# Optimization experiments

Hardware: AMD Instinct MI355X
Metric: run time of the kernel (lower is better)

The kernel has to match this reference:

```python
import jax, jax.numpy as jnp
import numpy as np

N_NODES = 100000


def _add_self_loops(edge_index, n):
    loop = jnp.arange(n, dtype=edge_index.dtype)
    src = jnp.concatenate([edge_index[0], loop])
    dst = jnp.concatenate([edge_index[1], loop])
    return src, dst


def gcn_conv(x, edge_index, W, b):
    # x: [N, Fin], edge_index: [2, E]; PyG GCNConv with add_self_loops + symmetric norm
    n = x.shape[0]
    src, dst = _add_self_loops(edge_index, n)
    # degree of augmented graph (counting incoming edges at dst, weight 1)
    deg = jax.ops.segment_sum(jnp.ones_like(dst, dtype=x.dtype), dst, num_segments=n)
    dinv = jnp.where(deg > 0, jax.lax.rsqrt(deg), 0.0)
    norm = dinv[src] * dinv[dst]                      # [E+N]
    h = x @ W                                         # [N, Fout] (transform first: Fout small)
    msg = h[src] * norm[:, None]                      # gather + scale
    out = jax.ops.segment_sum(msg, dst, num_segments=n)  # scatter-add
    return out + b


def setup_inputs() -> dict:
    key = jax.random.key(0)
    k1, k2, k3, k4, k5, k6 = jax.random.split(key, 6)
    F_in, H, C = 512, 16, 40
    x = jax.random.normal(k1, (N_NODES, F_in), dtype=jnp.float32)
    edge_index = jax.random.randint(k2, (2, 3200000), 0, N_NODES, dtype=jnp.int64)
    s1 = 1.0 / np.sqrt(F_in)
    s2 = 1.0 / np.sqrt(H)
    W1 = jax.random.uniform(k3, (F_in, H), jnp.float32, -s1, s1)
    b1 = jax.random.uniform(k4, (H,), jnp.float32, -s1, s1)
    W2 = jax.random.uniform(k5, (H, C), jnp.float32, -s2, s2)
    b2 = jax.random.uniform(k6, (C,), jnp.float32, -s2, s2)
    return {"x": x, "edge_index": edge_index, "W1": W1, "b1": b1, "W2": W2, "b2": b2}


def reference(x, edge_index, W1, b1, W2, b2):
    h = gcn_conv(x, edge_index, W1, b1)
    h = jax.nn.relu(h)
    # F.dropout(training=False) -> identity at inference
    h = gcn_conv(h, edge_index, W2, b2)
    return jax.nn.log_softmax(h, axis=1)
```

## Files before the change

kernel.cpp:

```cpp
#include <hip/hip_runtime.h>

#define N_NODES 100000
#define N_EDGES 3200000
#define FIN 512
#define FH 16
#define FC 40
#define NB_N ((N_NODES + 255) / 256)
#define NBKT 391
#define NBLK_P 256
#define CHUNK (N_EDGES / NBLK_P)


__global__ __launch_bounds__(256) void kA1(const int* __restrict__ dst,
                                           int* __restrict__ H) {
  __shared__ int h[NBKT];
  int t = threadIdx.x;
  for (int i = t; i < NBKT; i += 256) h[i] = 0;
  __syncthreads();
  int base = blockIdx.x * CHUNK;
  for (int i = t; i < CHUNK; i += 256) atomicAdd(&h[dst[base + i] >> 8], 1);
  __syncthreads();
  for (int i = t; i < NBKT; i += 256) H[blockIdx.x * NBKT + i] = h[i];
}


__global__ __launch_bounds__(256) void kA2(const int* __restrict__ H,
                                           int* __restrict__ P,
                                           int* __restrict__ T) {
  __shared__ int s[256];
  int t = threadIdx.x, b = blockIdx.x;
  int v = H[t * NBKT + b];
  s[t] = v;
  __syncthreads();
  for (int d = 1; d < 256; d <<= 1) {
    int x = (t >= d) ? s[t - d] : 0;
    __syncthreads();
    s[t] += x;
    __syncthreads();
  }
  P[t * NBKT + b] = s[t] - v;
  if (t == 255) T[b] = s[t];
}


__global__ __launch_bounds__(512) void kA3s(const int* __restrict__ T,
                                            int* __restrict__ Base,
                                            int* __restrict__ off) {
  __shared__ int s[512];
  int t = threadIdx.x;
  int v = (t < NBKT) ? T[t] : 0;
  s[t] = v;
  __syncthreads();
  for (int d = 1; d < 512; d <<= 1) {
    int x = (t >= d) ? s[t - d] : 0;
    __syncthreads();
    s[t] += x;
    __syncthreads();
  }
  if (t < NBKT) Base[t] = s[t] - v;
  if (t == 0) off[N_NODES] = N_EDGES;
}


__global__ __launch_bounds__(256) void kA3(const int* __restrict__ ei,
                                           const int* __restrict__ Base,
                                           const int* __restrict__ P,
                                           int* __restrict__ stage) {
  __shared__ int cur[NBKT];
  int t = threadIdx.x, blk = blockIdx.x;
  for (int i = t; i < NBKT; i += 256) cur[i] = Base[i] + P[blk * NBKT + i];
  __syncthreads();
  int base = blk * CHUNK;
  for (int i = t; i < CHUNK; i += 256) {
    int s = ei[base + i];
    int d = ei[N_EDGES + base + i];
    int slot = atomicAdd(&cur[d >> 8], 1);
    stage[slot] = s | ((d & 255) << 17);
  }
}


__global__ __launch_bounds__(256) void kB(const int* __restrict__ stage,
                                          const int* __restrict__ Base,
                                          const int* __restrict__ T,
                                          int* __restrict__ off,
                                          int* __restrict__ csr,
                                          float* __restrict__ dinv) {
  __shared__ int hist[256], cursor[256], sc[256];
  int t = threadIdx.x, b = blockIdx.x;
  int base = Base[b], cnt = T[b];
  hist[t] = 0;
  __syncthreads();
  for (int i = t; i < cnt; i += 256) atomicAdd(&hist[stage[base + i] >> 17], 1);
  __syncthreads();
  int c = hist[t];
  sc[t] = c;
  __syncthreads();
  for (int d = 1; d < 256; d <<= 1) {
    int x = (t >= d) ? sc[t - d] : 0;
    __syncthreads();
    sc[t] += x;
    __syncthreads();
  }
  int excl = sc[t] - c;
  int node = b * 256 + t;
  if (node < N_NODES) {
    off[node] = base + excl;
    dinv[node] = rsqrtf((float)(c + 1));
  }
  cursor[t] = excl;
  __syncthreads();
  for (int i = t; i < cnt; i += 256) {
    int pk = stage[base + i];
    int slot = atomicAdd(&cursor[pk >> 17], 1);
    csr[base + slot] = pk & 0x1FFFF;
  }
}


__global__ __launch_bounds__(256) void k_gemm1(const float* __restrict__ x,
                                               const float* __restrict__ W1,
                                               const float* __restrict__ dinv,
                                               float* __restrict__ p1) {
  __shared__ float xs[256 * 36];
  const int t = threadIdx.x;
  const int row0 = blockIdx.x * 256;
  const int row = row0 + t;
  float acc[FH];
#pragma unroll
  for (int c = 0; c < FH; c++) acc[c] = 0.0f;

  for (int kc = 0; kc < FIN; kc += 32) {
    float4 ld[8];
#pragma unroll
    for (int i = 0; i < 8; i++) {
      int idx = t + 256 * i;
      int r = idx >> 3, c4 = idx & 7;
      int gr = row0 + r;
      ld[i] = (gr < N_NODES)
                  ? *(const float4*)(x + (size_t)gr * FIN + kc + c4 * 4)
                  : make_float4(0.f, 0.f, 0.f, 0.f);
    }
    __syncthreads();
#pragma unroll
    for (int i = 0; i < 8; i++) {
      int idx = t + 256 * i;
      int r = idx >> 3, c4 = idx & 7;
      *(float4*)(&xs[r * 36 + c4 * 4]) = ld[i];
    }
    __syncthreads();
    float4 xr[8];
#pragma unroll
    for (int q = 0; q < 8; q++) xr[q] = *(const float4*)(&xs[t * 36 + q * 4]);
    const float4* w4 = (const float4*)(W1 + (size_t)kc * FH);
#pragma unroll
    for (int k = 0; k < 32; k++) {
      float xv = ((const float*)xr)[k];
      float4 wa = w4[k * 4 + 0], wb = w4[k * 4 + 1];
      float4 wc = w4[k * 4 + 2], wd = w4[k * 4 + 3];
      acc[0] = fmaf(xv, wa.x, acc[0]);   acc[1] = fmaf(xv, wa.y, acc[1]);
      acc[2] = fmaf(xv, wa.z, acc[2]);   acc[3] = fmaf(xv, wa.w, acc[3]);
      acc[4] = fmaf(xv, wb.x, acc[4]);   acc[5] = fmaf(xv, wb.y, acc[5]);
      acc[6] = fmaf(xv, wb.z, acc[6]);   acc[7] = fmaf(xv, wb.w, acc[7]);
      acc[8] = fmaf(xv, wc.x, acc[8]);   acc[9] = fmaf(xv, wc.y, acc[9]);
      acc[10] = fmaf(xv, wc.z, acc[10]); acc[11] = fmaf(xv, wc.w, acc[11]);
      acc[12] = fmaf(xv, wd.x, acc[12]); acc[13] = fmaf(xv, wd.y, acc[13]);
      acc[14] = fmaf(xv, wd.z, acc[14]); acc[15] = fmaf(xv, wd.w, acc[15]);
    }
  }

  if (row < N_NODES) {
    float dv = dinv[row];
#pragma unroll
    for (int c = 0; c < FH; c++) acc[c] *= dv;
#pragma unroll
    for (int q = 0; q < 4; q++)
      *(float4*)(p1 + (size_t)row * FH + q * 4) = ((const float4*)acc)[q];
  }
}


__global__ __launch_bounds__(256) void k_gather1(const int* __restrict__ off,
                                                 const int* __restrict__ csr,
                                                 const float* __restrict__ p1,
                                                 const float* __restrict__ dinv,
                                                 const float* __restrict__ b1,
                                                 float* __restrict__ q) {
  int lane = threadIdx.x & 63;
  int node = blockIdx.x * 4 + (threadIdx.x >> 6);
  int start = off[node];
  int end = off[node + 1];
  int slot = lane >> 2, comp = lane & 3;
  float4 acc = make_float4(0.f, 0.f, 0.f, 0.f);
  if (slot == 0)
    acc = *(const float4*)(p1 + (size_t)node * FH + comp * 4);
  for (int base = start; base < end; base += 16) {
    int e = base + slot;
    if (e < end) {
      int s = csr[e];
      float4 v = *(const float4*)(p1 + (size_t)s * FH + comp * 4);
      acc.x += v.x; acc.y += v.y; acc.z += v.z; acc.w += v.w;
    }
  }
#pragma unroll
  for (int m = 4; m <= 32; m <<= 1) {
    acc.x += __shfl_xor(acc.x, m);
    acc.y += __shfl_xor(acc.y, m);
    acc.z += __shfl_xor(acc.z, m);
    acc.w += __shfl_xor(acc.w, m);
  }
  float dv = dinv[node];
  if (lane < 4) {
    float4 bb = *(const float4*)(b1 + lane * 4);
    float4 r;
    r.x = fmaxf(fmaf(acc.x, dv, bb.x), 0.f) * dv;
    r.y = fmaxf(fmaf(acc.y, dv, bb.y), 0.f) * dv;
    r.z = fmaxf(fmaf(acc.z, dv, bb.z), 0.f) * dv;
    r.w = fmaxf(fmaf(acc.w, dv, bb.w), 0.f) * dv;
    *(float4*)(q + (size_t)node * FH + lane * 4) = r;
  }
}


__global__ __launch_bounds__(256) void k_gather2(const int* __restrict__ off,
                                                 const int* __restrict__ csr,
                                                 const float* __restrict__ q,
                                                 const float* __restrict__ dinv,
                                                 const float* __restrict__ W2,
                                                 const float* __restrict__ b2,
                                                 float* __restrict__ out) {
  int lane = threadIdx.x & 63;
  int node = blockIdx.x * 4 + (threadIdx.x >> 6);
  int start = off[node];
  int end = off[node + 1];
  int slot = lane >> 2, comp = lane & 3;
  float4 acc = make_float4(0.f, 0.f, 0.f, 0.f);
  if (slot == 0)
    acc = *(const float4*)(q + (size_t)node * FH + comp * 4);
  for (int base = start; base < end; base += 16) {
    int e = base + slot;
    if (e < end) {
      int s = csr[e];
      float4 v = *(const float4*)(q + (size_t)s * FH + comp * 4);
      acc.x += v.x; acc.y += v.y; acc.z += v.z; acc.w += v.w;
    }
  }
#pragma unroll
  for (int m = 4; m <= 32; m <<= 1) {
    acc.x += __shfl_xor(acc.x, m);
    acc.y += __shfl_xor(acc.y, m);
    acc.z += __shfl_xor(acc.z, m);
    acc.w += __shfl_xor(acc.w, m);
  }
  float dv = dinv[node];
  acc.x *= dv; acc.y *= dv; acc.z *= dv; acc.w *= dv;
  float t16[16];
  t16[comp * 4 + 0] = acc.x; t16[comp * 4 + 1] = acc.y;
  t16[comp * 4 + 2] = acc.z; t16[comp * 4 + 3] = acc.w;
#pragma unroll
  for (int m = 1; m <= 3; m++) {
    int oc = comp ^ m;
    t16[oc * 4 + 0] = __shfl_xor(acc.x, m);
    t16[oc * 4 + 1] = __shfl_xor(acc.y, m);
    t16[oc * 4 + 2] = __shfl_xor(acc.z, m);
    t16[oc * 4 + 3] = __shfl_xor(acc.w, m);
  }
  float z = -1e30f;
  if (lane < FC) {
    z = b2[lane];
#pragma unroll
    for (int k = 0; k < FH; k++) z = fmaf(t16[k], W2[k * FC + lane], z);
  }
  float mx = z;
#pragma unroll
  for (int d = 1; d < 64; d <<= 1) mx = fmaxf(mx, __shfl_xor(mx, d));
  float ex = (lane < FC) ? __expf(z - mx) : 0.f;
#pragma unroll
  for (int d = 1; d < 64; d <<= 1) ex += __shfl_xor(ex, d);
  float l = __logf(ex) + mx;
  if (lane < FC) out[(size_t)node * FC + lane] = z - l;
}


extern "C" void kernel_launch(void* const* d_in, const int* in_sizes, int n_in,
                              void* d_out, int out_size, void* d_ws, size_t ws_size,
                              hipStream_t stream) {
  const float* x  = (const float*)d_in[0];
  const int*   ei = (const int*)d_in[1];
  const float* W1 = (const float*)d_in[2];
  const float* b1 = (const float*)d_in[3];
  const float* W2 = (const float*)d_in[4];
  const float* b2 = (const float*)d_in[5];
  float* out = (float*)d_out;

  int* wsi  = (int*)d_ws;
  int* H    = wsi;
  int* P    = H + 100096;
  int* T    = P + 100096;
  int* Base = T + 512;
  int* off  = Base + 512;
  int* csr  = off + 100352;
  int* stage = csr + 3200000;
  float* dinv = (float*)(stage + 3200000);
  float* p1 = (float*)stage;
  float* q  = p1 + 1600000;

  kA1 <<<NBLK_P, 256, 0, stream>>>(ei + N_EDGES, H);
  kA2 <<<NBKT,   256, 0, stream>>>(H, P, T);
  kA3s<<<1,      512, 0, stream>>>(T, Base, off);
  kA3 <<<NBLK_P, 256, 0, stream>>>(ei, Base, P, stage);
  kB  <<<NBKT,   256, 0, stream>>>(stage, Base, T, off, csr, dinv);
  k_gemm1  <<<NB_N, 256, 0, stream>>>(x, W1, dinv, p1);
  k_gather1<<<N_NODES / 4, 256, 0, stream>>>(off, csr, p1, dinv, b1, q);
  k_gather2<<<N_NODES / 4, 256, 0, stream>>>(off, csr, q, dinv, W2, b2, out);
}
```

Before: 578.7 us.

## Replace full CSR build with bucketed staging and shared-memory atomic aggregation

```diff
diff --git a/kernel.cpp b/kernel.cpp
--- a/kernel.cpp
+++ b/kernel.cpp
@@ -6,9 +6,11 @@
 #define FH 16
 #define FC 40
 #define NB_N ((N_NODES + 255) / 256)
-#define NBKT 391
+#define BKT_SZ 128
+#define NBKT ((N_NODES + BKT_SZ - 1) / BKT_SZ)
 #define NBLK_P 256
 #define CHUNK (N_EDGES / NBLK_P)
+#define ACC_STRIDE 17
 
 
 __global__ __launch_bounds__(256) void kA1(const int* __restrict__ dst,
@@ -17,8 +19,14 @@
   int t = threadIdx.x;
   for (int i = t; i < NBKT; i += 256) h[i] = 0;
   __syncthreads();
-  int base = blockIdx.x * CHUNK;
-  for (int i = t; i < CHUNK; i += 256) atomicAdd(&h[dst[base + i] >> 8], 1);
+  const int4* d4 = (const int4*)(dst + blockIdx.x * CHUNK);
+  for (int i = t; i < CHUNK / 4; i += 256) {
+    int4 v = d4[i];
+    atomicAdd(&h[v.x >> 7], 1);
+    atomicAdd(&h[v.y >> 7], 1);
+    atomicAdd(&h[v.z >> 7], 1);
+    atomicAdd(&h[v.w >> 7], 1);
+  }
   __syncthreads();
   for (int i = t; i < NBKT; i += 256) H[blockIdx.x * NBKT + i] = h[i];
 }
@@ -26,7 +34,7 @@
 
 __global__ __launch_bounds__(256) void kA2(const int* __restrict__ H,
                                            int* __restrict__ P,
-                                           int* __restrict__ T) {
+                                           int* __restrict__ Tt) {
   __shared__ int s[256];
   int t = threadIdx.x, b = blockIdx.x;
   int v = H[t * NBKT + b];
@@ -39,26 +47,24 @@
     __syncthreads();
   }
   P[t * NBKT + b] = s[t] - v;
-  if (t == 255) T[b] = s[t];
-}
-
-
-__global__ __launch_bounds__(512) void kA3s(const int* __restrict__ T,
-                                            int* __restrict__ Base,
-                                            int* __restrict__ off) {
-  __shared__ int s[512];
+  if (t == 255) Tt[b] = s[t];
+}
+
+
+__global__ __launch_bounds__(1024) void kA3s(const int* __restrict__ Tt,
+                                             int* __restrict__ Base) {
+  __shared__ int s[1024];
   int t = threadIdx.x;
-  int v = (t < NBKT) ? T[t] : 0;
+  int v = (t < NBKT) ? Tt[t] : 0;
   s[t] = v;
   __syncthreads();
-  for (int d = 1; d < 512; d <<= 1) {
+  for (int d = 1; d < 1024; d <<= 1) {
     int x = (t >= d) ? s[t - d] : 0;
     __syncthreads();
     s[t] += x;
     __syncthreads();
   }
   if (t < NBKT) Base[t] = s[t] - v;
-  if (t == 0) off[N_NODES] = N_EDGES;
 }
 
 
@@ -71,50 +77,32 @@
   for (int i = t; i < NBKT; i += 256) cur[i] = Base[i] + P[blk * NBKT + i];
   __syncthreads();
   int base = blk * CHUNK;
-  for (int i = t; i < CHUNK; i += 256) {
-    int s = ei[base + i];
-    int d = ei[N_EDGES + base + i];
-    int slot = atomicAdd(&cur[d >> 8], 1);
-    stage[slot] = s | ((d & 255) << 17);
-  }
-}
-
-
-__global__ __launch_bounds__(256) void kB(const int* __restrict__ stage,
+  const int4* s4 = (const int4*)(ei + base);
+  const int4* d4 = (const int4*)(ei + N_EDGES + base);
+  for (int i = t; i < CHUNK / 4; i += 256) {
+    int4 sv = s4[i], dv = d4[i];
+    int slot;
+    slot = atomicAdd(&cur[dv.x >> 7], 1); stage[slot] = sv.x | ((dv.x & 127) << 17);
+    slot = atomicAdd(&cur[dv.y >> 7], 1); stage[slot] = sv.y | ((dv.y & 127) << 17);
+    slot = atomicAdd(&cur[dv.z >> 7], 1); stage[slot] = sv.z | ((dv.z & 127) << 17);
+    slot = atomicAdd(&cur[dv.w >> 7], 1); stage[slot] = sv.w | ((dv.w & 127) << 17);
+  }
+}
+
+
+__global__ __launch_bounds__(256) void kC(const int* __restrict__ stage,
                                           const int* __restrict__ Base,
-                                          const int* __restrict__ T,
-                                          int* __restrict__ off,
-                                          int* __restrict__ csr,
+                                          const int* __restrict__ Tt,
                                           float* __restrict__ dinv) {
-  __shared__ int hist[256], cursor[256], sc[256];
+  __shared__ int h[BKT_SZ];
   int t = threadIdx.x, b = blockIdx.x;
-  int base = Base[b], cnt = T[b];
-  hist[t] = 0;
-  __syncthreads();
-  for (int i = t; i < cnt; i += 256) atomicAdd(&hist[stage[base + i] >> 17], 1);
-  __syncthreads();
-  int c = hist[t];
-  sc[t] = c;
-  __syncthreads();
-  for (int d = 1; d < 256; d <<= 1) {
-    int x = (t >= d) ? sc[t - d] : 0;
-    __syncthreads();
-    sc[t] += x;
-    __syncthreads();
-  }
-  int excl = sc[t] - c;
-  int node = b * 256 + t;
-  if (node < N_NODES) {
-    off[node] = base + excl;
-    dinv[node] = rsqrtf((float)(c + 1));
-  }
-  cursor[t] = excl;
-  __syncthreads();
-  for (int i = t; i < cnt; i += 256) {
-    int pk = stage[base + i];
-    int slot = atomicAdd(&cursor[pk >> 17], 1);
-    csr[base + slot] = pk & 0x1FFFF;
-  }
+  if (t < BKT_SZ) h[t] = 0;
+  __syncthreads();
+  int base = Base[b], cnt = Tt[b];
+  for (int i = t; i < cnt; i += 256) atomicAdd(&h[(stage[base + i] >> 17) & 127], 1);
+  __syncthreads();
+  int node = b * BKT_SZ + t;
+  if (t < BKT_SZ && node < N_NODES) dinv[node] = rsqrtf((float)(h[t] + 1));
 }
 
 
@@ -180,105 +168,113 @@
 }
 
 
-__global__ __launch_bounds__(256) void k_gather1(const int* __restrict__ off,
-                                                 const int* __restrict__ csr,
-                                                 const float* __restrict__ p1,
-                                                 const float* __restrict__ dinv,
-                                                 const float* __restrict__ b1,
-                                                 float* __restrict__ q) {
-  int lane = threadIdx.x & 63;
-  int node = blockIdx.x * 4 + (threadIdx.x >> 6);
-  int start = off[node];
-  int end = off[node + 1];
-  int slot = lane >> 2, comp = lane & 3;
-  float4 acc = make_float4(0.f, 0.f, 0.f, 0.f);
-  if (slot == 0)
-    acc = *(const float4*)(p1 + (size_t)node * FH + comp * 4);
-  for (int base = start; base < end; base += 16) {
-    int e = base + slot;
-    if (e < end) {
-      int s = csr[e];
-      float4 v = *(const float4*)(p1 + (size_t)s * FH + comp * 4);
-      acc.x += v.x; acc.y += v.y; acc.z += v.z; acc.w += v.w;
+__global__ __launch_bounds__(256) void kG1(const int* __restrict__ stage,
+                                           const int* __restrict__ Base,
+                                           const int* __restrict__ Tt,
+                                           const float* __restrict__ p1,
+                                           const float* __restrict__ dinv,
+                                           const float* __restrict__ b1,
+                                           float* __restrict__ q) {
+  __shared__ float acc[BKT_SZ * ACC_STRIDE];
+  int t = threadIdx.x, b = blockIdx.x;
+  for (int i = t; i < BKT_SZ * ACC_STRIDE; i += 256) acc[i] = 0.f;
+  __syncthreads();
+  int base = Base[b], cnt = Tt[b];
+  int comp = t & 3;
+  for (int i = (t >> 2); i < cnt; i += 64) {
+    int pk = stage[base + i];
+    int src = pk & 0x1FFFF;
+    int dl = (pk >> 17) & 127;
+    float4 v = *(const float4*)(p1 + (size_t)src * FH + comp * 4);
+    float* a = &acc[dl * ACC_STRIDE + comp * 4];
+    atomicAdd(a + 0, v.x);
+    atomicAdd(a + 1, v.y);
+    atomicAdd(a + 2, v.z);
+    atomicAdd(a + 3, v.w);
+  }
+  __syncthreads();
+  for (int idx = t; idx < BKT_SZ * 4; idx += 256) {
+    int dl = idx >> 2, c = idx & 3;
+    int node = b * BKT_SZ + dl;
+    if (node >= N_NODES) continue;
+    float dv = dinv[node];
+    float4 sv = *(const float4*)(p1 + (size_t)node * FH + c * 4);
+    float4 bb = *(const float4*)(b1 + c * 4);
+    const float* a = &acc[dl * ACC_STRIDE + c * 4];
+    float4 r;
+    r.x = fmaxf(fmaf(a[0] + sv.x, dv, bb.x), 0.f) * dv;
+    r.y = fmaxf(fmaf(a[1] + sv.y, dv, bb.y), 0.f) * dv;
+    r.z = fmaxf(fmaf(a[2] + sv.z, dv, bb.z), 0.f) * dv;
+    r.w = fmaxf(fmaf(a[3] + sv.w, dv, bb.w), 0.f) * dv;
+    *(float4*)(q + (size_t)node * FH + c * 4) = r;
+  }
+}
+
+
+__global__ __launch_bounds__(256) void kG2(const int* __restrict__ stage,
+                                           const int* __restrict__ Base,
+                                           const int* __restrict__ Tt,
+                                           const float* __restrict__ q,
+                                           const float* __restrict__ dinv,
+                                           const float* __restrict__ W2,
+                                           const float* __restrict__ b2,
+                                           float* __restrict__ out) {
+  __shared__ float acc[BKT_SZ * ACC_STRIDE];
+  int t = threadIdx.x, b = blockIdx.x;
+  for (int i = t; i < BKT_SZ * ACC_STRIDE; i += 256) acc[i] = 0.f;
+  __syncthreads();
+  int base = Base[b], cnt = Tt[b];
+  int comp = t & 3;
+  for (int i = (t >> 2); i < cnt; i += 64) {
+    int pk = stage[base + i];
+    int src = pk & 0x1FFFF;
+    int dl = (pk >> 17) & 127;
+    float4 v = *(const float4*)(q + (size_t)src * FH + comp * 4);
+    float* a = &acc[dl * ACC_STRIDE + comp * 4];
+    atomicAdd(a + 0, v.x);
+    atomicAdd(a + 1, v.y);
+    atomicAdd(a + 2, v.z);
+    atomicAdd(a + 3, v.w);
+  }
+  __syncthreads();
+  for (int idx = t; idx < BKT_SZ * 4; idx += 256) {
+    int dl = idx >> 2, c = idx & 3;
+    int node = b * BKT_SZ + dl;
+    if (node < N_NODES) {
+      float4 sv = *(const float4*)(q + (size_t)node * FH + c * 4);
+      float* a = &acc[dl * ACC_STRIDE + c * 4];
+      a[0] += sv.x; a[1] += sv.y; a[2] += sv.z; a[3] += sv.w;
     }
   }
-#pragma unroll
-  for (int m = 4; m <= 32; m <<= 1) {
-    acc.x += __shfl_xor(acc.x, m);
-    acc.y += __shfl_xor(acc.y, m);
-    acc.z += __shfl_xor(acc.z, m);
-    acc.w += __shfl_xor(acc.w, m);
-  }
-  float dv = dinv[node];
-  if (lane < 4) {
-    float4 bb = *(const float4*)(b1 + lane * 4);
-    float4 r;
-    r.x = fmaxf(fmaf(acc.x, dv, bb.x), 0.f) * dv;
-    r.y = fmaxf(fmaf(acc.y, dv, bb.y), 0.f) * dv;
-    r.z = fmaxf(fmaf(acc.z, dv, bb.z), 0.f) * dv;
-    r.w = fmaxf(fmaf(acc.w, dv, bb.w), 0.f) * dv;
-    *(float4*)(q + (size_t)node * FH + lane * 4) = r;
-  }
-}
-
-
-__global__ __launch_bounds__(256) void k_gather2(const int* __restrict__ off,
-                                                 const int* __restrict__ csr,
-                                                 const float* __restrict__ q,
-                                                 const float* __restrict__ dinv,
-                                                 const float* __restrict__ W2,
-                                                 const float* __restrict__ b2,
-                                                 float* __restrict__ out) {
-  int lane = threadIdx.x & 63;
-  int node = blockIdx.x * 4 + (threadIdx.x >> 6);
-  int start = off[node];
-  int end = off[node + 1];
-  int slot = lane >> 2, comp = lane & 3;
-  float4 acc = make_float4(0.f, 0.f, 0.f, 0.f);
-  if (slot == 0)
-    acc = *(const float4*)(q + (size_t)node * FH + comp * 4);
-  for (int base = start; base < end; base += 16) {
-    int e = base + slot;
-    if (e < end) {
-      int s = csr[e];
-      float4 v = *(const float4*)(q + (size_t)s * FH + comp * 4);
-      acc.x += v.x; acc.y += v.y; acc.z += v.z; acc.w += v.w;
-    }
-  }
-#pragma unroll
-  for (int m = 4; m <= 32; m <<= 1) {
-    acc.x += __shfl_xor(acc.x, m);
-    acc.y += __shfl_xor(acc.y, m);
-    acc.z += __shfl_xor(acc.z, m);
-    acc.w += __shfl_xor(acc.w, m);
-  }
-  float dv = dinv[node];
-  acc.x *= dv; acc.y *= dv; acc.z *= dv; acc.w *= dv;
-  float t16[16];
-  t16[comp * 4 + 0] = acc.x; t16[comp * 4 + 1] = acc.y;
-  t16[comp * 4 + 2] = acc.z; t16[comp * 4 + 3] = acc.w;
-#pragma unroll
-  for (int m = 1; m <= 3; m++) {
-    int oc = comp ^ m;
-    t16[oc * 4 + 0] = __shfl_xor(acc.x, m);
-    t16[oc * 4 + 1] = __shfl_xor(acc.y, m);
-    t16[oc * 4 + 2] = __shfl_xor(acc.z, m);
-    t16[oc * 4 + 3] = __shfl_xor(acc.w, m);
-  }
-  float z = -1e30f;
+  __syncthreads();
+  int lane = t & 63, wv = t >> 6;
+  float w2c[FH];
+#pragma unroll
+  for (int k = 0; k < FH; k++) w2c[k] = 0.f;
+  float bc = 0.f;
   if (lane < FC) {
-    z = b2[lane];
-#pragma unroll
-    for (int k = 0; k < FH; k++) z = fmaf(t16[k], W2[k * FC + lane], z);
-  }
-  float mx = z;
-#pragma unroll
-  for (int d = 1; d < 64; d <<= 1) mx = fmaxf(mx, __shfl_xor(mx, d));
-  float ex = (lane < FC) ? __expf(z - mx) : 0.f;
-#pragma unroll
-  for (int d = 1; d < 64; d <<= 1) ex += __shfl_xor(ex, d);
-  float l = __logf(ex) + mx;
-  if (lane < FC) out[(size_t)node * FC + lane] = z - l;
+#pragma unroll
+    for (int k = 0; k < FH; k++) w2c[k] = W2[k * FC + lane];
+    bc = b2[lane];
+  }
+  for (int dl = wv; dl < BKT_SZ; dl += 4) {
+    int node = b * BKT_SZ + dl;
+    if (node >= N_NODES) continue;
+    float dv = dinv[node];
+    const float* ar = &acc[dl * ACC_STRIDE];
+    float z = bc;
+#pragma unroll
+    for (int k = 0; k < FH; k++) z = fmaf(ar[k] * dv, w2c[k], z);
+    float zz = (lane < FC) ? z : -1e30f;
+    float mx = zz;
+#pragma unroll
+    for (int d = 1; d < 64; d <<= 1) mx = fmaxf(mx, __shfl_xor(mx, d));
+    float ex = (lane < FC) ? __expf(zz - mx) : 0.f;
+#pragma unroll
+    for (int d = 1; d < 64; d <<= 1) ex += __shfl_xor(ex, d);
+    float l = __logf(ex) + mx;
+    if (lane < FC) out[(size_t)node * FC + lane] = zz - l;
+  }
 }
 
 
@@ -293,24 +289,22 @@
   const float* b2 = (const float*)d_in[5];
   float* out = (float*)d_out;
 
-  int* wsi  = (int*)d_ws;
-  int* H    = wsi;
-  int* P    = H + 100096;
-  int* T    = P + 100096;
-  int* Base = T + 512;
-  int* off  = Base + 512;
-  int* csr  = off + 100352;
-  int* stage = csr + 3200000;
+  int* wsi   = (int*)d_ws;
+  int* H     = wsi;
+  int* P     = H + 200192;
+  int* Tt    = P + 200192;
+  int* Base  = Tt + 800;
+  int* stage = Base + 800;
   float* dinv = (float*)(stage + 3200000);
-  float* p1 = (float*)stage;
-  float* q  = p1 + 1600000;
-
-  kA1 <<<NBLK_P, 256, 0, stream>>>(ei + N_EDGES, H);
-  kA2 <<<NBKT,   256, 0, stream>>>(H, P, T);
-  kA3s<<<1,      512, 0, stream>>>(T, Base, off);
-  kA3 <<<NBLK_P, 256, 0, stream>>>(ei, Base, P, stage);
-  kB  <<<NBKT,   256, 0, stream>>>(stage, Base, T, off, csr, dinv);
-  k_gemm1  <<<NB_N, 256, 0, stream>>>(x, W1, dinv, p1);
-  k_gather1<<<N_NODES / 4, 256, 0, stream>>>(off, csr, p1, dinv, b1, q);
-  k_gather2<<<N_NODES / 4, 256, 0, stream>>>(off, csr, q, dinv, W2, b2, out);
-}
+  float* p1  = dinv + 100352;
+  float* q   = p1 + 1600000;
+
+  kA1 <<<NBLK_P, 256,  0, stream>>>(ei + N_EDGES, H);
+  kA2 <<<NBKT,   256,  0, stream>>>(H, P, Tt);
+  kA3s<<<1,      1024, 0, stream>>>(Tt, Base);
+  kA3 <<<NBLK_P, 256,  0, stream>>>(ei, Base, P, stage);
+  kC  <<<NBKT,   256,  0, stream>>>(stage, Base, Tt, dinv);
+  k_gemm1<<<NB_N, 256, 0, stream>>>(x, W1, dinv, p1);
+  kG1 <<<NBKT,   256,  0, stream>>>(stage, Base, Tt, p1, dinv, b1, q);
+  kG2 <<<NBKT,   256,  0, stream>>>(stage, Base, Tt, q, dinv, W2, b2, out);
+}
```

Result: slower. 1.116 ms (+92.8%).
